# Performance work log

Hardware: AMD Instinct MI355X
Metric: run time of the kernel (lower is better)

## Reference

```python
import jax, jax.numpy as jnp
import numpy as np

FILTER_LENGTH = 1024
HOP_LENGTH = 512
CUTOFF = FILTER_LENGTH // 2 + 1  # 513
PAD_AMOUNT = FILTER_LENGTH // 2  # 512


def _make_forward_basis():
    # DFT matrix rows (real stacked over imag, up to Nyquist), windowed by periodic Hann.
    fb = np.fft.fft(np.eye(FILTER_LENGTH))
    fb = np.vstack([np.real(fb[:CUTOFF, :]), np.imag(fb[:CUTOFF, :])])  # [1026, 1024]
    n = np.arange(FILTER_LENGTH)
    # scipy get_window('hann', N, fftbins=True) == periodic Hann
    win = 0.5 * (1.0 - np.cos(2.0 * np.pi * n / FILTER_LENGTH))
    basis = (fb * win[None, :]).astype(np.float32)
    return basis[:, None, :]  # [out_ch=1026, in_ch=1, k=1024]


def setup_inputs() -> dict:
    key = jax.random.key(0)
    audio = jax.random.normal(key, (15360000,), dtype=jnp.float32)
    forward_basis = jnp.asarray(_make_forward_basis())
    return {"audio": audio, "forward_basis": forward_basis}


def reference(audio, forward_basis):
    # [L] -> [1, 1, L + 2*pad] with reflect padding
    x = jnp.pad(audio, (PAD_AMOUNT, PAD_AMOUNT), mode="reflect")[None, None, :]
    # Strided conv1d == windowed DFT per frame; output [1, 1026, n_frames]
    ft = jax.lax.conv_general_dilated(
        x,
        forward_basis,
        window_strides=(HOP_LENGTH,),
        padding="VALID",
        dimension_numbers=("NCH", "OIH", "NCH"),
    )
    real = ft[:, :CUTOFF, :]
    imag = ft[:, CUTOFF:, :]
    return real * real + imag * imag  # power spectrum [1, 513, n_frames]
```

## Files before the change

kernel.cpp:

```cpp
#include <hip/hip_runtime.h>

#define L_AUDIO 15360000
#define PADLEN  15361024
#define FRAMES  30001
#define CHP     513
#define NBAS    (1026*1024)

#define BM  256
#define BNP 128
#define BK  64
#define NKT 16
#define NCB 5
#define NFB 118
#define NWG (NFB*NCB)

typedef __attribute__((ext_vector_type(8))) short short8;
typedef __attribute__((ext_vector_type(4))) float f32x4;

__device__ __forceinline__ unsigned short f2bf(float f) {
    unsigned int u = __float_as_uint(f);
    u += 0x7fffu + ((u >> 16) & 1u);
    return (unsigned short)(u >> 16);
}

__global__ __launch_bounds__(256) void prep_pad_k(const float* __restrict__ a,
                                                  unsigned short* __restrict__ pad) {
    long i = (long)blockIdx.x * blockDim.x + threadIdx.x;
    long p0 = i * 4;
    if (p0 >= 512 && p0 + 4 <= 512 + L_AUDIO) {
        const float4 v = *reinterpret_cast<const float4*>(a + (p0 - 512));
        ushort4 o;
        o.x = f2bf(v.x); o.y = f2bf(v.y); o.z = f2bf(v.z); o.w = f2bf(v.w);
        *reinterpret_cast<ushort4*>(pad + p0) = o;
    } else {
        for (int j = 0; j < 4; ++j) {
            long p = p0 + j;
            long src = p - 512;
            if (p < 512) src = 512 - p;
            else if (src >= L_AUDIO) src = 2L*L_AUDIO - 2 - src;
            pad[p] = f2bf(a[src]);
        }
    }
}

__global__ __launch_bounds__(256) void prep_bas_k(const float* __restrict__ b,
                                                  unsigned short* __restrict__ o) {
    long i = (long)blockIdx.x * blockDim.x + threadIdx.x;
    const float4 v = *reinterpret_cast<const float4*>(b + i * 4);
    ushort4 u;
    u.x = f2bf(v.x); u.y = f2bf(v.y); u.z = f2bf(v.z); u.w = f2bf(v.w);
    *reinterpret_cast<ushort4*>(o + i * 4) = u;
}

__global__ __launch_bounds__(512, 2) void stft_gemm(const unsigned short* __restrict__ pad,
                                                    const unsigned short* __restrict__ bas,
                                                    float* __restrict__ out) {
    __shared__ unsigned short lsA[2][BM * BK];
    __shared__ unsigned short lsB[2][BM * BK];

    const int tid  = threadIdx.x;
    const int w    = tid >> 6;
    const int lane = tid & 63;
    const int l15  = lane & 15;
    const int lk   = lane >> 4;
    const int wm   = w >> 2;
    const int wn   = w & 3;

    const int orig = blockIdx.x;
    const int xcd  = orig & 7;
    const int lid  = orig >> 3;
    const int wg   = (xcd < 6 ? xcd * 74 : 6 * 74 + (xcd - 6) * 73) + lid;
    const int fb   = wg / NCB;
    const int cb   = wg - fb * NCB;
    const long t0  = (long)fb * BM;
    const int  c0  = cb * BNP;

    const unsigned short* aS[4];
    const unsigned short* bS[4];
    #pragma unroll
    for (int j = 0; j < 4; ++j) {
        const int c   = j * 512 + tid;
        const int row = c >> 3;
        const int sc  = (c & 7) ^ (row & 7);
        long tf = t0 + row; if (tf > FRAMES - 1) tf = FRAMES - 1;
        aS[j] = pad + tf * 512 + sc * 8;
        const int g = row >> 4;
        int ch = c0 + (g >> 1) * 16 + (row & 15); if (ch > 512) ch = 512;
        const long brow = (g & 1) ? (long)(513 + ch) : (long)ch;
        bS[j] = bas + brow * 1024 + sc * 8;
    }

    f32x4 acc[8][4];
    #pragma unroll
    for (int a = 0; a < 8; ++a)
        #pragma unroll
        for (int b = 0; b < 4; ++b)
            acc[a][b] = (f32x4){0.f, 0.f, 0.f, 0.f};

    const int wmBase = wm * 128;
    const int wnBase = wn * 64;

#define GLD(dst, src) __builtin_amdgcn_global_load_lds( \
        (const __attribute__((address_space(1))) unsigned int*)(src), \
        (__attribute__((address_space(3))) unsigned int*)(dst), 16, 0, 0)

#define LDSREAD(basePtr, r, S) \
    (*reinterpret_cast<const short8*>(reinterpret_cast<const char*>(basePtr) \
        + (r) * 128 + ((((S) * 4 + lk) ^ ((r) & 7)) << 4)))

#define PHASE_RA(MQ, S) do { _Pragma("unroll") \
    for (int j = 0; j < 4; ++j) { \
        const int r = wmBase + ((MQ) * 4 + j) * 16 + l15; \
        af[j] = LDSREAD(curA, r, S); } } while (0)

#define PHASE_RB(S) do { _Pragma("unroll") \
    for (int b = 0; b < 4; ++b) { \
        const int r = wnBase + b * 16 + l15; \
        bf[b] = LDSREAD(curB, r, S); } } while (0)

#define PHASE_MFMA(MQ) do { \
    __builtin_amdgcn_s_setprio(1); \
    _Pragma("unroll") for (int b = 0; b < 4; ++b) \
        _Pragma("unroll") for (int j = 0; j < 4; ++j) \
            acc[(MQ)*4+j][b] = __builtin_amdgcn_mfma_f32_16x16x32_bf16( \
                af[j], bf[b], acc[(MQ)*4+j][b], 0, 0, 0); \
    __builtin_amdgcn_s_setprio(0); } while (0)

    #pragma unroll
    for (int j = 0; j < 4; ++j) {
        GLD(&lsA[0][(j * 512 + tid) * 8], aS[j]);
        GLD(&lsB[0][(j * 512 + tid) * 8], bS[j]);
    }

    short8 af[4], bf[4];

    for (int t = 0; t < NKT; ++t) {
        unsigned short* curA = lsA[t & 1];
        unsigned short* curB = lsB[t & 1];
        unsigned short* nxtA = lsA[(t & 1) ^ 1];
        unsigned short* nxtB = lsB[(t & 1) ^ 1];
        const bool more = (t + 1 < NKT);
        const int ko = (t + 1) * BK;

        if (more) { GLD(&nxtA[(0*512+tid)*8], aS[0]+ko); GLD(&nxtA[(1*512+tid)*8], aS[1]+ko); }
        if (more) asm volatile("s_waitcnt vmcnt(2)" ::: "memory");
        else      asm volatile("s_waitcnt vmcnt(0)" ::: "memory");
        __builtin_amdgcn_s_barrier();

        PHASE_RA(0, 0); PHASE_RB(0);
        if (more) { GLD(&nxtA[(2*512+tid)*8], aS[2]+ko); GLD(&nxtA[(3*512+tid)*8], aS[3]+ko); }
        __builtin_amdgcn_s_barrier();
        PHASE_MFMA(0);
        __builtin_amdgcn_s_barrier();

        PHASE_RA(1, 0);
        if (more) { GLD(&nxtB[(0*512+tid)*8], bS[0]+ko); GLD(&nxtB[(1*512+tid)*8], bS[1]+ko); }
        __builtin_amdgcn_s_barrier();
        PHASE_MFMA(1);
        __builtin_amdgcn_s_barrier();

        PHASE_RA(0, 1); PHASE_RB(1);
        if (more) { GLD(&nxtB[(2*512+tid)*8], bS[2]+ko); GLD(&nxtB[(3*512+tid)*8], bS[3]+ko); }
        __builtin_amdgcn_s_barrier();
        PHASE_MFMA(0);
        __builtin_amdgcn_s_barrier();

        PHASE_RA(1, 1);
        __builtin_amdgcn_s_barrier();
        PHASE_MFMA(1);
        __builtin_amdgcn_s_barrier();
    }

    const int tb = (int)t0 + wmBase;
    #pragma unroll
    for (int a = 0; a < 8; ++a) {
        #pragma unroll
        for (int q = 0; q < 2; ++q) {
            const int ch = c0 + wn * 32 + q * 16 + l15;
            if (ch >= CHP) continue;
            const long ob = (long)ch * FRAMES;
            const int tv = tb + a * 16 + lk * 4;
            const f32x4 re = acc[a][q * 2];
            const f32x4 im = acc[a][q * 2 + 1];
            if (tv + 3 < FRAMES) {
                #pragma unroll
                for (int r = 0; r < 4; ++r)
                    out[ob + tv + r] = re[r] * re[r] + im[r] * im[r];
            } else {
                #pragma unroll
                for (int r = 0; r < 4; ++r)
                    if (tv + r < FRAMES)
                        out[ob + tv + r] = re[r] * re[r] + im[r] * im[r];
            }
        }
    }
}

extern "C" void kernel_launch(void* const* d_in, const int* in_sizes, int n_in,
                              void* d_out, int out_size, void* d_ws, size_t ws_size,
                              hipStream_t stream) {
    const float* audio = (const float*)d_in[0];
    const float* basis = (const float*)d_in[1];
    float* out = (float*)d_out;

    unsigned short* pad = (unsigned short*)d_ws;
    unsigned short* bas = pad + PADLEN;

    prep_pad_k<<<PADLEN / 4 / 256, 256, 0, stream>>>(audio, pad);
    prep_bas_k<<<NBAS / 4 / 256, 256, 0, stream>>>(basis, bas);

    stft_gemm<<<NWG, 512, 0, stream>>>(pad, bas, out);
}
```

Before: 111.3 us.

## Replace phased barrier schedule with bulk prefetch and two-barrier K loop

Removes the four-phase interleaved schedule, which split LDS reads, global-to-LDS prefetches and MFMA groups across eight barriers per K tile. Now all eight prefetch loads for the next tile are issued at the top of the loop, the kernel waits for the current tile, and a single barrier precedes a straight loop of LDS reads and MFMAs over both K sub-steps. It is meant to cut barrier count and sync stalls and give the compiler freedom to interleave LDS reads with MFMAs. In exchange it drops the explicit setprio hints and the fine-grained overlap of loads with compute, and may raise register pressure.

```diff
diff --git a/kernel.cpp b/kernel.cpp
--- a/kernel.cpp
+++ b/kernel.cpp
@@ -108,31 +108,11 @@
     (*reinterpret_cast<const short8*>(reinterpret_cast<const char*>(basePtr) \
         + (r) * 128 + ((((S) * 4 + lk) ^ ((r) & 7)) << 4)))
 
-#define PHASE_RA(MQ, S) do { _Pragma("unroll") \
-    for (int j = 0; j < 4; ++j) { \
-        const int r = wmBase + ((MQ) * 4 + j) * 16 + l15; \
-        af[j] = LDSREAD(curA, r, S); } } while (0)
-
-#define PHASE_RB(S) do { _Pragma("unroll") \
-    for (int b = 0; b < 4; ++b) { \
-        const int r = wnBase + b * 16 + l15; \
-        bf[b] = LDSREAD(curB, r, S); } } while (0)
-
-#define PHASE_MFMA(MQ) do { \
-    __builtin_amdgcn_s_setprio(1); \
-    _Pragma("unroll") for (int b = 0; b < 4; ++b) \
-        _Pragma("unroll") for (int j = 0; j < 4; ++j) \
-            acc[(MQ)*4+j][b] = __builtin_amdgcn_mfma_f32_16x16x32_bf16( \
-                af[j], bf[b], acc[(MQ)*4+j][b], 0, 0, 0); \
-    __builtin_amdgcn_s_setprio(0); } while (0)
-
     #pragma unroll
     for (int j = 0; j < 4; ++j) {
         GLD(&lsA[0][(j * 512 + tid) * 8], aS[j]);
         GLD(&lsB[0][(j * 512 + tid) * 8], bS[j]);
     }
-
-    short8 af[4], bf[4];
 
     for (int t = 0; t < NKT; ++t) {
         unsigned short* curA = lsA[t & 1];
@@ -142,33 +122,38 @@
         const bool more = (t + 1 < NKT);
         const int ko = (t + 1) * BK;
 
-        if (more) { GLD(&nxtA[(0*512+tid)*8], aS[0]+ko); GLD(&nxtA[(1*512+tid)*8], aS[1]+ko); }
-        if (more) asm volatile("s_waitcnt vmcnt(2)" ::: "memory");
-        else      asm volatile("s_waitcnt vmcnt(0)" ::: "memory");
+        if (more) {
+            #pragma unroll
+            for (int j = 0; j < 4; ++j) {
+                GLD(&nxtA[(j * 512 + tid) * 8], aS[j] + ko);
+                GLD(&nxtB[(j * 512 + tid) * 8], bS[j] + ko);
+            }
+            asm volatile("s_waitcnt vmcnt(8)" ::: "memory");
+        } else {
+            asm volatile("s_waitcnt vmcnt(0)" ::: "memory");
+        }
         __builtin_amdgcn_s_barrier();
+        asm volatile("" ::: "memory");
 
-        PHASE_RA(0, 0); PHASE_RB(0);
-        if (more) { GLD(&nxtA[(2*512+tid)*8], aS[2]+ko); GLD(&nxtA[(3*512+tid)*8], aS[3]+ko); }
+        #pragma unroll
+        for (int S = 0; S < 2; ++S) {
+            short8 bf[4];
+            #pragma unroll
+            for (int b = 0; b < 4; ++b)
+                bf[b] = LDSREAD(curB, wnBase + b * 16 + l15, S);
+            #pragma unroll
+            for (int mq = 0; mq < 8; ++mq) {
+                short8 af = LDSREAD(curA, wmBase + mq * 16 + l15, S);
+                #pragma unroll
+                for (int b = 0; b < 4; ++b)
+                    acc[mq][b] = __builtin_amdgcn_mfma_f32_16x16x32_bf16(
+                        af, bf[b], acc[mq][b], 0, 0, 0);
+            }
+        }
+
+        asm volatile("" ::: "memory");
         __builtin_amdgcn_s_barrier();
-        PHASE_MFMA(0);
-        __builtin_amdgcn_s_barrier();
-
-        PHASE_RA(1, 0);
-        if (more) { GLD(&nxtB[(0*512+tid)*8], bS[0]+ko); GLD(&nxtB[(1*512+tid)*8], bS[1]+ko); }
-        __builtin_amdgcn_s_barrier();
-        PHASE_MFMA(1);
-        __builtin_amdgcn_s_barrier();
-
-        PHASE_RA(0, 1); PHASE_RB(1);
-        if (more) { GLD(&nxtB[(2*512+tid)*8], bS[2]+ko); GLD(&nxtB[(3*512+tid)*8], bS[3]+ko); }
-        __builtin_amdgcn_s_barrier();
-        PHASE_MFMA(0);
-        __builtin_amdgcn_s_barrier();
-
-        PHASE_RA(1, 1);
-        __builtin_amdgcn_s_barrier();
-        PHASE_MFMA(1);
-        __builtin_amdgcn_s_barrier();
+        asm volatile("" ::: "memory");
     }
 
     const int tb = (int)t0 + wmBase;
```

New measurement: 114.7 us. +3.1%, slower.
